# Kernel tuning notes

Hardware: AMD Instinct MI355X
Metric: run time of the kernel (lower is better)

## Reference

```python
import jax, jax.numpy as jnp
import numpy as np

B, N, C = 16, 1024, 768
H, HD = 9, 64  # num_active_heads, head_dim


def setup_inputs() -> dict:
    key = jax.random.key(0)
    ks = jax.random.split(key, 5)
    x = jax.random.normal(ks[0], (B, N, C), dtype=jnp.float32)
    qkv_w = jax.random.normal(ks[1], (3 * H * HD, C), dtype=jnp.float32) * (1.0 / np.sqrt(C))
    qkv_b = jax.random.normal(ks[2], (3 * H * HD,), dtype=jnp.float32) * 0.02
    proj_w = jax.random.normal(ks[3], (C, H * HD), dtype=jnp.float32) * (1.0 / np.sqrt(H * HD))
    proj_b = jax.random.normal(ks[4], (C,), dtype=jnp.float32) * 0.02
    return {"x": x, "qkv_w": qkv_w, "qkv_b": qkv_b, "proj_w": proj_w, "proj_b": proj_b}


def reference(x, qkv_w, qkv_b, proj_w, proj_b):
    b, n, c = x.shape
    # qkv projection: [B,N,3*H*HD] -> [3,B,H,N,HD]
    qkv = (x @ qkv_w.T + qkv_b).reshape(b, n, 3, H, HD).transpose(2, 0, 3, 1, 4)
    q, k, v = qkv[0], qkv[1], qkv[2]
    scale = HD ** -0.5
    attn = jnp.einsum('bhqd,bhkd->bhqk', q, k) * scale  # [B,H,N,N]
    attn = jax.nn.softmax(attn, axis=-1)
    out = jnp.einsum('bhqk,bhkd->bhqd', attn, v)  # [B,H,N,HD]
    out = out.transpose(0, 2, 1, 3).reshape(b, n, H * HD)
    return out @ proj_w.T + proj_b
```

## Files before the change

### kernel.cpp

```cpp
#include <hip/hip_runtime.h>


typedef _Float16 f16x8 __attribute__((ext_vector_type(8)));
typedef _Float16 f16x4 __attribute__((ext_vector_type(4)));
typedef __fp16   h16x2 __attribute__((ext_vector_type(2)));
typedef float    f32x4 __attribute__((ext_vector_type(4)));

#define MFMA16(a, b, c) __builtin_amdgcn_mfma_f32_16x16x32_f16(a, b, c, 0, 0, 0)

__device__ __forceinline__ void gld16(const _Float16* g, _Float16* l) {
  __builtin_amdgcn_global_load_lds((const __attribute__((address_space(1))) void*)g,
                                   (__attribute__((address_space(3))) void*)l, 16, 0, 0);
}

__global__ __launch_bounds__(256) void cvt_swz(const float* __restrict__ src,
                                               _Float16* __restrict__ dst,
                                               int rows_src, int cpr, int total) {
  const int g = blockIdx.x * 256 + threadIdx.x;
  if (g >= total) return;
  const int row = g / cpr;
  const int c = g - row * cpr;
  const int L = cpr * 8;
  const int pos = (c & ~7) | ((c ^ row) & 7);
  union { f16x8 v; h16x2 h[4]; } u;
  if (row < rows_src) {
    const float4 a = *(const float4*)(src + row * L + c * 8);
    const float4 b = *(const float4*)(src + row * L + c * 8 + 4);
    u.h[0] = __builtin_amdgcn_cvt_pkrtz(a.x, a.y);
    u.h[1] = __builtin_amdgcn_cvt_pkrtz(a.z, a.w);
    u.h[2] = __builtin_amdgcn_cvt_pkrtz(b.x, b.y);
    u.h[3] = __builtin_amdgcn_cvt_pkrtz(b.z, b.w);
  } else {
    u.v = (f16x8){};
  }
  *(f16x8*)(dst + row * L + pos * 8) = u.v;
}

__global__ __launch_bounds__(256, 4) void gemm1_qkv(const _Float16* __restrict__ A,
                                                    const _Float16* __restrict__ Bw,
                                                    const float* __restrict__ bias,
                                                    _Float16* __restrict__ Qo,
                                                    _Float16* __restrict__ Ko,
                                                    _Float16* __restrict__ Vt) {
  __shared__ __align__(16) _Float16 As[128 * 64];
  __shared__ __align__(16) _Float16 Bs[128 * 64];
  const int tid = threadIdx.x;
  const int wave = tid >> 6, lane = tid & 63;
  const int lo = lane & 15, hi = lane >> 4;
  const int wm = (wave >> 1) * 64, wn = (wave & 1) * 64;
  const int m0 = blockIdx.x * 128, n0 = blockIdx.y * 128;
  f32x4 acc[4][4] = {};
  for (int k0 = 0; k0 < 768; k0 += 64) {
    __syncthreads();
    #pragma unroll
    for (int j = 0; j < 4; ++j) {
      const int seg = wave * 4 + j;
      const int gr = seg * 8 + (lane >> 3), gc = (lane & 7) << 3;
      gld16(A + (m0 + gr) * 768 + k0 + gc, As + seg * 512);
      gld16(Bw + (n0 + gr) * 768 + k0 + gc, Bs + seg * 512);
    }
    __syncthreads();
    #pragma unroll
    for (int ks = 0; ks < 2; ++ks) {
      f16x8 af[4], bf[4];
      const int p = ((ks * 4 + hi) ^ (lo & 7)) << 3;
      #pragma unroll
      for (int t = 0; t < 4; ++t) {
        af[t] = *(const f16x8*)(As + (wm + t * 16 + lo) * 64 + p);
        bf[t] = *(const f16x8*)(Bs + (wn + t * 16 + lo) * 64 + p);
      }
      #pragma unroll
      for (int mt = 0; mt < 4; ++mt)
        #pragma unroll
        for (int nt = 0; nt < 4; ++nt)
          acc[mt][nt] = MFMA16(af[mt], bf[nt], acc[mt][nt]);
    }
  }
  const int b = m0 >> 10;
  const int nrbase = (m0 & 1023) + wm;
  #pragma unroll
  for (int nt = 0; nt < 4; ++nt) {
    const int n = n0 + wn + nt * 16 + lo;
    if (n < 1728) {
      const float bv = bias[n];
      const int t3 = n / 576;
      const int rem = n - t3 * 576;
      const int hh = rem >> 6, d = rem & 63;
      const int bh16 = (b * 9 + hh) << 16;
      if (t3 == 2) {
        _Float16* dv = Vt + bh16 + d * 1024;
        #pragma unroll
        for (int mt = 0; mt < 4; ++mt) {
          const int nr = nrbase + mt * 16 + hi * 4;
          const int c = nr >> 3;
          const int pos = (c & ~7) | ((c ^ d) & 7);
          union { f16x4 v; h16x2 h[2]; } u;
          u.h[0] = __builtin_amdgcn_cvt_pkrtz(acc[mt][nt][0] + bv, acc[mt][nt][1] + bv);
          u.h[1] = __builtin_amdgcn_cvt_pkrtz(acc[mt][nt][2] + bv, acc[mt][nt][3] + bv);
          *(f16x4*)(dv + pos * 8 + (nr & 7)) = u.v;
        }
      } else if (t3 == 1) {
        _Float16* dk = Ko + bh16;
        const int ch = d >> 3, dl = d & 7;
        #pragma unroll
        for (int mt = 0; mt < 4; ++mt) {
          const int nr = nrbase + mt * 16 + hi * 4;
          #pragma unroll
          for (int i = 0; i < 4; ++i) {
            const int t = nr + i;
            dk[t * 64 + ((ch ^ (t & 7)) << 3) + dl] = (_Float16)(acc[mt][nt][i] + bv);
          }
        }
      } else {
        _Float16* dq = Qo + bh16 + d;
        #pragma unroll
        for (int mt = 0; mt < 4; ++mt) {
          const int nr = nrbase + mt * 16 + hi * 4;
          #pragma unroll
          for (int i = 0; i < 4; ++i)
            dq[(nr + i) * 64] = (_Float16)(acc[mt][nt][i] + bv);
        }
      }
    }
  }
}

__global__ __launch_bounds__(256, 4) void attn_fused(const _Float16* __restrict__ Qg,
                                                     const _Float16* __restrict__ Kg,
                                                     const _Float16* __restrict__ Vtg,
                                                     _Float16* __restrict__ Og) {
  __shared__ __align__(16) _Float16 Ks[2][64 * 64];
  __shared__ __align__(16) _Float16 Vts[2][64 * 64];
  __shared__ __align__(16) _Float16 Ps[4][16 * 64];
  const int tid = threadIdx.x;
  const int wave = tid >> 6, lane = tid & 63;
  const int lo = lane & 15, hi = lane >> 4;
  const int bid = blockIdx.x;
  const int xcd = bid & 7, idx = bid >> 3;
  const int bh = xcd * 18 + (idx >> 4);
  const int q0 = (idx & 15) << 6;
  const _Float16* Qp  = Qg + (bh << 16);
  const _Float16* Kp  = Kg + (bh << 16);
  const _Float16* Vtp = Vtg + (bh << 16);

  auto issue = [&](int t0, int nb) {
    #pragma unroll
    for (int j = 0; j < 2; ++j) {
      const int seg = wave * 2 + j;
      gld16(Kp + (t0 + seg * 8 + (lane >> 3)) * 64 + ((lane & 7) << 3), &Ks[nb][seg * 512]);
      gld16(Vtp + (seg * 8 + (lane >> 3)) * 1024 + t0 + ((lane & 7) << 3), &Vts[nb][seg * 512]);
    }
  };

  issue(0, 0);

  f16x8 qf[2];
  const _Float16* qrow = Qp + (q0 + wave * 16 + lo) * 64;
  qf[0] = *(const f16x8*)(qrow + hi * 8);
  qf[1] = *(const f16x8*)(qrow + (4 + hi) * 8);

  float m_run = -1e30f, l_run = 0.f;
  f32x4 accO[4] = {};
  const float cs = 0.125f * 1.44269504f;
  _Float16* Pw = Ps[wave];

  auto compute = [&](int cb) {
    const _Float16* Kc = Ks[cb];
    const _Float16* Vc = Vts[cb];
    f32x4 sacc[4] = {};
    #pragma unroll
    for (int tt = 0; tt < 4; ++tt)
      #pragma unroll
      for (int ks = 0; ks < 2; ++ks) {
        const f16x8 kf = *(const f16x8*)(Kc + (tt * 16 + lo) * 64 + (((ks * 4 + hi) ^ (lo & 7)) << 3));
        sacc[tt] = MFMA16(kf, qf[ks], sacc[tt]);
      }
    float rmax = -1e30f;
    #pragma unroll
    for (int tt = 0; tt < 4; ++tt)
      rmax = fmaxf(rmax, fmaxf(fmaxf(sacc[tt][0], sacc[tt][1]), fmaxf(sacc[tt][2], sacc[tt][3])));
    rmax = fmaxf(rmax, __shfl_xor(rmax, 16, 64));
    rmax = fmaxf(rmax, __shfl_xor(rmax, 32, 64));
    const float mnew = fmaxf(m_run, rmax * cs);
    const float alpha = __builtin_amdgcn_exp2f(m_run - mnew);
    float rsum = 0.f;
    #pragma unroll
    for (int tt = 0; tt < 4; ++tt) {
      const float p0 = __builtin_amdgcn_exp2f(fmaf(sacc[tt][0], cs, -mnew));
      const float p1 = __builtin_amdgcn_exp2f(fmaf(sacc[tt][1], cs, -mnew));
      const float p2 = __builtin_amdgcn_exp2f(fmaf(sacc[tt][2], cs, -mnew));
      const float p3 = __builtin_amdgcn_exp2f(fmaf(sacc[tt][3], cs, -mnew));
      rsum += (p0 + p1) + (p2 + p3);
      union { f16x4 v; h16x2 h[2]; } u;
      u.h[0] = __builtin_amdgcn_cvt_pkrtz(p0, p1);
      u.h[1] = __builtin_amdgcn_cvt_pkrtz(p2, p3);
      const int c = 2 * tt + (hi >> 1);
      *(f16x4*)(Pw + lo * 64 + (((c ^ lo) & 7) << 3) + ((hi & 1) << 2)) = u.v;
    }
    rsum += __shfl_xor(rsum, 16, 64);
    rsum += __shfl_xor(rsum, 32, 64);
    l_run = l_run * alpha + rsum;
    m_run = mnew;
    #pragma unroll
    for (int dt = 0; dt < 4; ++dt) accO[dt] *= alpha;

    #pragma unroll
    for (int ks2 = 0; ks2 < 2; ++ks2) {
      const int c = 4 * ks2 + hi;
      const f16x8 pf = *(const f16x8*)(Pw + lo * 64 + (((c ^ lo) & 7) << 3));
      #pragma unroll
      for (int dt = 0; dt < 4; ++dt) {
        const int dd = dt * 16 + lo;
        const f16x8 vf = *(const f16x8*)(Vc + dd * 64 + (((c ^ dd) & 7) << 3));
        accO[dt] = MFMA16(vf, pf, accO[dt]);
      }
    }
  };

  auto step = [&](int tnext0, int cb, bool pre) {
    if (pre) {
      issue(tnext0, cb ^ 1);
      asm volatile("s_waitcnt vmcnt(4)" ::: "memory");
    } else {
      asm volatile("s_waitcnt vmcnt(0)" ::: "memory");
    }
    __builtin_amdgcn_sched_barrier(0);
    __builtin_amdgcn_s_barrier();
    compute(cb);
    __builtin_amdgcn_sched_barrier(0);
    __builtin_amdgcn_s_barrier();
  };

  #pragma unroll 1
  for (int it = 0; it < 7; ++it) {
    step((2 * it + 1) << 6, 0, true);
    step((2 * it + 2) << 6, 1, true);
  }
  step(15 << 6, 0, true);
  step(0, 1, false);

  const float inv = 1.f / l_run;
  const int b = bh / 9, hh = bh - b * 9;
  const int rq = (b << 10) + q0 + wave * 16 + lo;
  #pragma unroll
  for (int dt = 0; dt < 4; ++dt) {
    union { f16x4 v; h16x2 h[2]; } u;
    u.h[0] = __builtin_amdgcn_cvt_pkrtz(accO[dt][0] * inv, accO[dt][1] * inv);
    u.h[1] = __builtin_amdgcn_cvt_pkrtz(accO[dt][2] * inv, accO[dt][3] * inv);
    const int c = hh * 8 + dt * 2 + (hi >> 1);
    const int pos = (c & ~7) | ((c ^ rq) & 7);
    *(f16x4*)(Og + rq * 576 + pos * 8 + ((hi & 1) << 2)) = u.v;
  }
}

__global__ __launch_bounds__(256, 4) void gemm3_proj(const _Float16* __restrict__ A,
                                                     const _Float16* __restrict__ Bw,
                                                     const float* __restrict__ bias,
                                                     float* __restrict__ out) {
  __shared__ __align__(16) _Float16 As[128 * 64];
  __shared__ __align__(16) _Float16 Bs[128 * 64];
  const int tid = threadIdx.x;
  const int wave = tid >> 6, lane = tid & 63;
  const int lo = lane & 15, hi = lane >> 4;
  const int wm = (wave >> 1) * 64, wn = (wave & 1) * 64;
  const int m0 = blockIdx.x * 128, n0 = blockIdx.y * 128;
  f32x4 acc[4][4] = {};
  for (int k0 = 0; k0 < 576; k0 += 64) {
    __syncthreads();
    #pragma unroll
    for (int j = 0; j < 4; ++j) {
      const int seg = wave * 4 + j;
      const int gr = seg * 8 + (lane >> 3), gc = (lane & 7) << 3;
      gld16(A + (m0 + gr) * 576 + k0 + gc, As + seg * 512);
      gld16(Bw + (n0 + gr) * 576 + k0 + gc, Bs + seg * 512);
    }
    __syncthreads();
    #pragma unroll
    for (int ks = 0; ks < 2; ++ks) {
      f16x8 af[4], bf[4];
      const int p = ((ks * 4 + hi) ^ (lo & 7)) << 3;
      #pragma unroll
      for (int t = 0; t < 4; ++t) {
        af[t] = *(const f16x8*)(As + (wm + t * 16 + lo) * 64 + p);
        bf[t] = *(const f16x8*)(Bs + (wn + t * 16 + lo) * 64 + p);
      }
      #pragma unroll
      for (int mt = 0; mt < 4; ++mt)
        #pragma unroll
        for (int nt = 0; nt < 4; ++nt)
          acc[mt][nt] = MFMA16(af[mt], bf[nt], acc[mt][nt]);
    }
  }
  #pragma unroll
  for (int nt = 0; nt < 4; ++nt) {
    const int n = n0 + wn + nt * 16 + lo;
    const float bv = bias[n];
    #pragma unroll
    for (int mt = 0; mt < 4; ++mt) {
      const int mrow = m0 + wm + mt * 16 + hi * 4;
      #pragma unroll
      for (int i = 0; i < 4; ++i)
        out[(mrow + i) * 768 + n] = acc[mt][nt][i] + bv;
    }
  }
}

extern "C" void kernel_launch(void* const* d_in, const int* in_sizes, int n_in,
                              void* d_out, int out_size, void* d_ws, size_t ws_size,
                              hipStream_t stream) {
  const float* x      = (const float*)d_in[0];
  const float* qkv_w  = (const float*)d_in[1];
  const float* qkv_b  = (const float*)d_in[2];
  const float* proj_w = (const float*)d_in[3];
  const float* proj_b = (const float*)d_in[4];
  float* out = (float*)d_out;

  char* ws = (char*)d_ws;
  _Float16* x16 = (_Float16*)(ws + 0);
  _Float16* w1p = (_Float16*)(ws + 25165824);
  _Float16* w2h = (_Float16*)(ws + 27918336);
  _Float16* Qh  = (_Float16*)(ws + 28803072);
  _Float16* Kh  = (_Float16*)(ws + 47677440);
  _Float16* Vth = (_Float16*)(ws + 66551808);
  _Float16* Oh  = (_Float16*)(ws + 85426176);

  cvt_swz<<<6144, 256, 0, stream>>>(x, x16, 16384, 96, 16384 * 96);
  cvt_swz<<<672, 256, 0, stream>>>(qkv_w, w1p, 1728, 96, 1792 * 96);
  cvt_swz<<<216, 256, 0, stream>>>(proj_w, w2h, 768, 72, 768 * 72);
  gemm1_qkv<<<dim3(128, 14), 256, 0, stream>>>(x16, w1p, qkv_b, Qh, Kh, Vth);
  attn_fused<<<2304, 256, 0, stream>>>(Qh, Kh, Vth, Oh);
  gemm3_proj<<<dim3(128, 6), 256, 0, stream>>>(Oh, w2h, proj_b, out);
}
```

Measured before the change: 256.2 us.

## Process two 64-row query tiles per attention block to reuse K/V tiles

Each attention block now handles 128 query rows, as two independent 64-row groups per wave set, instead of 64. The K/V shared-memory tiles loaded per step are reused for both groups, halving the number of blocks and the total K/V global traffic. The cost is doubled accumulator and score registers per thread, which may reduce occupancy under the 4-blocks-per-SM launch bound, and fewer blocks in the grid. The shared P buffer is reused sequentially by the two groups.

```diff
diff --git a/kernel.cpp b/kernel.cpp
--- a/kernel.cpp
+++ b/kernel.cpp
@@ -137,8 +137,8 @@
   const int lo = lane & 15, hi = lane >> 4;
   const int bid = blockIdx.x;
   const int xcd = bid & 7, idx = bid >> 3;
-  const int bh = xcd * 18 + (idx >> 4);
-  const int q0 = (idx & 15) << 6;
+  const int bh = xcd * 18 + (idx >> 3);
+  const int q0 = (idx & 7) << 7;
   const _Float16* Qp  = Qg + (bh << 16);
   const _Float16* Kp  = Kg + (bh << 16);
   const _Float16* Vtp = Vtg + (bh << 16);
@@ -154,27 +154,21 @@
 
   issue(0, 0);
 
-  f16x8 qf[2];
-  const _Float16* qrow = Qp + (q0 + wave * 16 + lo) * 64;
-  qf[0] = *(const f16x8*)(qrow + hi * 8);
-  qf[1] = *(const f16x8*)(qrow + (4 + hi) * 8);
-
-  float m_run = -1e30f, l_run = 0.f;
-  f32x4 accO[4] = {};
+  f16x8 qf0[2], qf1[2];
+  const _Float16* qrow0 = Qp + (q0 + wave * 16 + lo) * 64;
+  const _Float16* qrow1 = qrow0 + 64 * 64;
+  qf0[0] = *(const f16x8*)(qrow0 + hi * 8);
+  qf0[1] = *(const f16x8*)(qrow0 + (4 + hi) * 8);
+  qf1[0] = *(const f16x8*)(qrow1 + hi * 8);
+  qf1[1] = *(const f16x8*)(qrow1 + (4 + hi) * 8);
+
+  float m0_ = -1e30f, l0_ = 0.f, m1_ = -1e30f, l1_ = 0.f;
+  f32x4 accO0[4] = {}, accO1[4] = {};
   const float cs = 0.125f * 1.44269504f;
   _Float16* Pw = Ps[wave];
 
-  auto compute = [&](int cb) {
-    const _Float16* Kc = Ks[cb];
-    const _Float16* Vc = Vts[cb];
-    f32x4 sacc[4] = {};
-    #pragma unroll
-    for (int tt = 0; tt < 4; ++tt)
-      #pragma unroll
-      for (int ks = 0; ks < 2; ++ks) {
-        const f16x8 kf = *(const f16x8*)(Kc + (tt * 16 + lo) * 64 + (((ks * 4 + hi) ^ (lo & 7)) << 3));
-        sacc[tt] = MFMA16(kf, qf[ks], sacc[tt]);
-      }
+  auto grp = [&](f32x4 (&sacc)[4], f32x4 (&accO)[4], float& m_run, float& l_run,
+                 const _Float16* Vc) {
     float rmax = -1e30f;
     #pragma unroll
     for (int tt = 0; tt < 4; ++tt)
@@ -203,7 +197,6 @@
     m_run = mnew;
     #pragma unroll
     for (int dt = 0; dt < 4; ++dt) accO[dt] *= alpha;
-
     #pragma unroll
     for (int ks2 = 0; ks2 < 2; ++ks2) {
       const int c = 4 * ks2 + hi;
@@ -215,6 +208,22 @@
         accO[dt] = MFMA16(vf, pf, accO[dt]);
       }
     }
+  };
+
+  auto compute = [&](int cb) {
+    const _Float16* Kc = Ks[cb];
+    const _Float16* Vc = Vts[cb];
+    f32x4 s0[4] = {}, s1[4] = {};
+    #pragma unroll
+    for (int tt = 0; tt < 4; ++tt)
+      #pragma unroll
+      for (int ks = 0; ks < 2; ++ks) {
+        const f16x8 kf = *(const f16x8*)(Kc + (tt * 16 + lo) * 64 + (((ks * 4 + hi) ^ (lo & 7)) << 3));
+        s0[tt] = MFMA16(kf, qf0[ks], s0[tt]);
+        s1[tt] = MFMA16(kf, qf1[ks], s1[tt]);
+      }
+    grp(s0, accO0, m0_, l0_, Vc);
+    grp(s1, accO1, m1_, l1_, Vc);
   };
 
   auto step = [&](int tnext0, int cb, bool pre) {
@@ -239,17 +248,32 @@
   step(15 << 6, 0, true);
   step(0, 1, false);
 
-  const float inv = 1.f / l_run;
   const int b = bh / 9, hh = bh - b * 9;
-  const int rq = (b << 10) + q0 + wave * 16 + lo;
-  #pragma unroll
-  for (int dt = 0; dt < 4; ++dt) {
-    union { f16x4 v; h16x2 h[2]; } u;
-    u.h[0] = __builtin_amdgcn_cvt_pkrtz(accO[dt][0] * inv, accO[dt][1] * inv);
-    u.h[1] = __builtin_amdgcn_cvt_pkrtz(accO[dt][2] * inv, accO[dt][3] * inv);
-    const int c = hh * 8 + dt * 2 + (hi >> 1);
-    const int pos = (c & ~7) | ((c ^ rq) & 7);
-    *(f16x4*)(Og + rq * 576 + pos * 8 + ((hi & 1) << 2)) = u.v;
+  {
+    const float inv = 1.f / l0_;
+    const int rq = (b << 10) + q0 + wave * 16 + lo;
+    #pragma unroll
+    for (int dt = 0; dt < 4; ++dt) {
+      union { f16x4 v; h16x2 h[2]; } u;
+      u.h[0] = __builtin_amdgcn_cvt_pkrtz(accO0[dt][0] * inv, accO0[dt][1] * inv);
+      u.h[1] = __builtin_amdgcn_cvt_pkrtz(accO0[dt][2] * inv, accO0[dt][3] * inv);
+      const int c = hh * 8 + dt * 2 + (hi >> 1);
+      const int pos = (c & ~7) | ((c ^ rq) & 7);
+      *(f16x4*)(Og + rq * 576 + pos * 8 + ((hi & 1) << 2)) = u.v;
+    }
+  }
+  {
+    const float inv = 1.f / l1_;
+    const int rq = (b << 10) + q0 + 64 + wave * 16 + lo;
+    #pragma unroll
+    for (int dt = 0; dt < 4; ++dt) {
+      union { f16x4 v; h16x2 h[2]; } u;
+      u.h[0] = __builtin_amdgcn_cvt_pkrtz(accO1[dt][0] * inv, accO1[dt][1] * inv);
+      u.h[1] = __builtin_amdgcn_cvt_pkrtz(accO1[dt][2] * inv, accO1[dt][3] * inv);
+      const int c = hh * 8 + dt * 2 + (hi >> 1);
+      const int pos = (c & ~7) | ((c ^ rq) & 7);
+      *(f16x4*)(Og + rq * 576 + pos * 8 + ((hi & 1) << 2)) = u.v;
+    }
   }
 }
 
@@ -328,6 +352,6 @@
   cvt_swz<<<672, 256, 0, stream>>>(qkv_w, w1p, 1728, 96, 1792 * 96);
   cvt_swz<<<216, 256, 0, stream>>>(proj_w, w2h, 768, 72, 768 * 72);
   gemm1_qkv<<<dim3(128, 14), 256, 0, stream>>>(x16, w1p, qkv_b, Qh, Kh, Vth);
-  attn_fused<<<2304, 256, 0, stream>>>(Qh, Kh, Vth, Oh);
+  attn_fused<<<1152, 256, 0, stream>>>(Qh, Kh, Vth, Oh);
   gemm3_proj<<<dim3(128, 6), 256, 0, stream>>>(Oh, w2h, proj_b, out);
 }
```

Result: slower. 406.4 us (+58.6%).

## Remap GEMM blocks per XCD and skip online-softmax rescale when max stable

Applied to the files above, without the earlier changes.

Both projection GEMMs now use a 1D grid whose block index is remapped so that each XCD handles a contiguous band of M tiles across all N tiles. The aim is better reuse of A-tile rows in that XCD's L2. The attention kernel now applies lazy rescaling: when no lane's new row max exceeds the running max by more than 8 (in log2 units), it keeps the old max and skips the exp2 alpha and the accumulator multiply. That saves ALU work per key tile, but unnormalized probabilities can grow up to 2^8, which is safe in fp32 yet raises fp16 range concerns for P.

```diff
diff --git a/kernel.cpp b/kernel.cpp
--- a/kernel.cpp
+++ b/kernel.cpp
@@ -48,7 +48,10 @@
   const int wave = tid >> 6, lane = tid & 63;
   const int lo = lane & 15, hi = lane >> 4;
   const int wm = (wave >> 1) * 64, wn = (wave & 1) * 64;
-  const int m0 = blockIdx.x * 128, n0 = blockIdx.y * 128;
+  const int g = blockIdx.x;
+  const int xcd = g & 7, i = g >> 3;
+  const int mt = i / 14, ntl = i - mt * 14;
+  const int m0 = (xcd * 16 + mt) * 128, n0 = ntl * 128;
   f32x4 acc[4][4] = {};
   for (int k0 = 0; k0 < 768; k0 += 64) {
     __syncthreads();
@@ -70,10 +73,10 @@
         bf[t] = *(const f16x8*)(Bs + (wn + t * 16 + lo) * 64 + p);
       }
       #pragma unroll
-      for (int mt = 0; mt < 4; ++mt)
+      for (int mt2 = 0; mt2 < 4; ++mt2)
         #pragma unroll
         for (int nt = 0; nt < 4; ++nt)
-          acc[mt][nt] = MFMA16(af[mt], bf[nt], acc[mt][nt]);
+          acc[mt2][nt] = MFMA16(af[mt2], bf[nt], acc[mt2][nt]);
     }
   }
   const int b = m0 >> 10;
@@ -90,35 +93,35 @@
       if (t3 == 2) {
         _Float16* dv = Vt + bh16 + d * 1024;
         #pragma unroll
-        for (int mt = 0; mt < 4; ++mt) {
-          const int nr = nrbase + mt * 16 + hi * 4;
+        for (int mt2 = 0; mt2 < 4; ++mt2) {
+          const int nr = nrbase + mt2 * 16 + hi * 4;
           const int c = nr >> 3;
           const int pos = (c & ~7) | ((c ^ d) & 7);
           union { f16x4 v; h16x2 h[2]; } u;
-          u.h[0] = __builtin_amdgcn_cvt_pkrtz(acc[mt][nt][0] + bv, acc[mt][nt][1] + bv);
-          u.h[1] = __builtin_amdgcn_cvt_pkrtz(acc[mt][nt][2] + bv, acc[mt][nt][3] + bv);
+          u.h[0] = __builtin_amdgcn_cvt_pkrtz(acc[mt2][nt][0] + bv, acc[mt2][nt][1] + bv);
+          u.h[1] = __builtin_amdgcn_cvt_pkrtz(acc[mt2][nt][2] + bv, acc[mt2][nt][3] + bv);
           *(f16x4*)(dv + pos * 8 + (nr & 7)) = u.v;
         }
       } else if (t3 == 1) {
         _Float16* dk = Ko + bh16;
         const int ch = d >> 3, dl = d & 7;
         #pragma unroll
-        for (int mt = 0; mt < 4; ++mt) {
-          const int nr = nrbase + mt * 16 + hi * 4;
+        for (int mt2 = 0; mt2 < 4; ++mt2) {
+          const int nr = nrbase + mt2 * 16 + hi * 4;
           #pragma unroll
-          for (int i = 0; i < 4; ++i) {
-            const int t = nr + i;
-            dk[t * 64 + ((ch ^ (t & 7)) << 3) + dl] = (_Float16)(acc[mt][nt][i] + bv);
+          for (int i2 = 0; i2 < 4; ++i2) {
+            const int t = nr + i2;
+            dk[t * 64 + ((ch ^ (t & 7)) << 3) + dl] = (_Float16)(acc[mt2][nt][i2] + bv);
           }
         }
       } else {
         _Float16* dq = Qo + bh16 + d;
         #pragma unroll
-        for (int mt = 0; mt < 4; ++mt) {
-          const int nr = nrbase + mt * 16 + hi * 4;
+        for (int mt2 = 0; mt2 < 4; ++mt2) {
+          const int nr = nrbase + mt2 * 16 + hi * 4;
           #pragma unroll
-          for (int i = 0; i < 4; ++i)
-            dq[(nr + i) * 64] = (_Float16)(acc[mt][nt][i] + bv);
+          for (int i2 = 0; i2 < 4; ++i2)
+            dq[(nr + i2) * 64] = (_Float16)(acc[mt2][nt][i2] + bv);
         }
       }
     }
@@ -181,8 +184,10 @@
       rmax = fmaxf(rmax, fmaxf(fmaxf(sacc[tt][0], sacc[tt][1]), fmaxf(sacc[tt][2], sacc[tt][3])));
     rmax = fmaxf(rmax, __shfl_xor(rmax, 16, 64));
     rmax = fmaxf(rmax, __shfl_xor(rmax, 32, 64));
-    const float mnew = fmaxf(m_run, rmax * cs);
-    const float alpha = __builtin_amdgcn_exp2f(m_run - mnew);
+    const float rs = rmax * cs;
+    const bool nsk = !__all(rs <= m_run + 8.f);
+    const float mnew = nsk ? fmaxf(m_run, rs) : m_run;
+    const float alpha = nsk ? __builtin_amdgcn_exp2f(m_run - mnew) : 1.f;
     float rsum = 0.f;
     #pragma unroll
     for (int tt = 0; tt < 4; ++tt) {
@@ -201,8 +206,10 @@
     rsum += __shfl_xor(rsum, 32, 64);
     l_run = l_run * alpha + rsum;
     m_run = mnew;
-    #pragma unroll
-    for (int dt = 0; dt < 4; ++dt) accO[dt] *= alpha;
+    if (nsk) {
+      #pragma unroll
+      for (int dt = 0; dt < 4; ++dt) accO[dt] *= alpha;
+    }
 
     #pragma unroll
     for (int ks2 = 0; ks2 < 2; ++ks2) {
@@ -263,7 +270,10 @@
   const int wave = tid >> 6, lane = tid & 63;
   const int lo = lane & 15, hi = lane >> 4;
   const int wm = (wave >> 1) * 64, wn = (wave & 1) * 64;
-  const int m0 = blockIdx.x * 128, n0 = blockIdx.y * 128;
+  const int g = blockIdx.x;
+  const int xcd = g & 7, i = g >> 3;
+  const int mt = i / 6, ntl = i - mt * 6;
+  const int m0 = (xcd * 16 + mt) * 128, n0 = ntl * 128;
   f32x4 acc[4][4] = {};
   for (int k0 = 0; k0 < 576; k0 += 64) {
     __syncthreads();
@@ -285,10 +295,10 @@
         bf[t] = *(const f16x8*)(Bs + (wn + t * 16 + lo) * 64 + p);
       }
       #pragma unroll
-      for (int mt = 0; mt < 4; ++mt)
+      for (int mt2 = 0; mt2 < 4; ++mt2)
         #pragma unroll
         for (int nt = 0; nt < 4; ++nt)
-          acc[mt][nt] = MFMA16(af[mt], bf[nt], acc[mt][nt]);
+          acc[mt2][nt] = MFMA16(af[mt2], bf[nt], acc[mt2][nt]);
     }
   }
   #pragma unroll
@@ -296,11 +306,11 @@
     const int n = n0 + wn + nt * 16 + lo;
     const float bv = bias[n];
     #pragma unroll
-    for (int mt = 0; mt < 4; ++mt) {
-      const int mrow = m0 + wm + mt * 16 + hi * 4;
-      #pragma unroll
-      for (int i = 0; i < 4; ++i)
-        out[(mrow + i) * 768 + n] = acc[mt][nt][i] + bv;
+    for (int mt2 = 0; mt2 < 4; ++mt2) {
+      const int mrow = m0 + wm + mt2 * 16 + hi * 4;
+      #pragma unroll
+      for (int i2 = 0; i2 < 4; ++i2)
+        out[(mrow + i2) * 768 + n] = acc[mt2][nt][i2] + bv;
     }
   }
 }
@@ -327,7 +337,7 @@
   cvt_swz<<<6144, 256, 0, stream>>>(x, x16, 16384, 96, 16384 * 96);
   cvt_swz<<<672, 256, 0, stream>>>(qkv_w, w1p, 1728, 96, 1792 * 96);
   cvt_swz<<<216, 256, 0, stream>>>(proj_w, w2h, 768, 72, 768 * 72);
-  gemm1_qkv<<<dim3(128, 14), 256, 0, stream>>>(x16, w1p, qkv_b, Qh, Kh, Vth);
+  gemm1_qkv<<<1792, 256, 0, stream>>>(x16, w1p, qkv_b, Qh, Kh, Vth);
   attn_fused<<<2304, 256, 0, stream>>>(Qh, Kh, Vth, Oh);
-  gemm3_proj<<<dim3(128, 6), 256, 0, stream>>>(Oh, w2h, proj_b, out);
-}
+  gemm3_proj<<<768, 256, 0, stream>>>(Oh, w2h, proj_b, out);
+}
```

Measured after the change: 247.4 us. -3.4%, faster.
